# Performance work log

Hardware: AMD Instinct MI355X
Metric: run time of the kernel (lower is better)

Reference implementation:

```python
import jax, jax.numpy as jnp
import numpy as np


def _spectral_norm(W, u):
    # W: [out, in] (1x1 conv weight flattened), u: [out]
    # one power-iteration step (torch does this under no_grad), then
    # sigma = u' @ W @ v with gradient flowing through W only.
    v = W.T @ u
    v = v / jnp.linalg.norm(v)
    u2 = W @ v
    u2 = u2 / jnp.linalg.norm(u2)
    v = jax.lax.stop_gradient(v)
    u2 = jax.lax.stop_gradient(u2)
    sigma = u2 @ (W @ v)
    return W / sigma


def setup_inputs() -> dict:
    key = jax.random.key(0)
    ks = jax.random.split(key, 8)
    B, C, H, W = 32, 512, 32, 32
    Cq = C // 8  # 64
    x = jax.random.normal(ks[0], (B, C, H, W), dtype=jnp.float32)
    s = 1.0 / np.sqrt(C)
    return {
        "x": x,
        "Wq": jax.random.normal(ks[1], (Cq, C), dtype=jnp.float32) * s,
        "bq": jnp.zeros((Cq,), dtype=jnp.float32),
        "uq": jax.random.normal(ks[2], (Cq,), dtype=jnp.float32),
        "Wk": jax.random.normal(ks[3], (Cq, C), dtype=jnp.float32) * s,
        "bk": jnp.zeros((Cq,), dtype=jnp.float32),
        "uk": jax.random.normal(ks[4], (Cq,), dtype=jnp.float32),
        "Wv": jax.random.normal(ks[5], (C, C), dtype=jnp.float32) * s,
        "bv": jnp.zeros((C,), dtype=jnp.float32),
        "uv": jax.random.normal(ks[6], (C,), dtype=jnp.float32),
        "gamma": jnp.float32(0.5),
    }


def reference(x, Wq, bq, uq, Wk, bk, uk, Wv, bv, uv, gamma):
    B, C, H, W = x.shape
    N = H * W
    f = x.reshape(B, C, N)                                   # [B,C,N]
    # 1x1 conv == channel matmul with spectral-normalized weights
    q = jnp.einsum('oc,bcn->bno', _spectral_norm(Wq, uq), f) + bq          # [B,N,Cq]
    k = jnp.einsum('oc,bcn->bon', _spectral_norm(Wk, uk), f) + bk[:, None]  # [B,Cq,N]
    v = jnp.einsum('oc,bcn->bon', _spectral_norm(Wv, uv), f) + bv[:, None]  # [B,C,N]
    qk = jnp.einsum('bno,bom->bnm', q, k)                    # [B,N,N], no 1/sqrt(d)
    attn = jax.nn.softmax(qk, axis=1)                        # softmax over QUERY axis (dim 1)
    o = jnp.einsum('bcn,bnm->bcm', v, attn).reshape(B, C, H, W)
    return gamma * o + x
```

## Files before the change

### kernel.cpp

```cpp
#include <hip/hip_runtime.h>
#include <hip/hip_bf16.h>

typedef __hip_bfloat16 bf16;
typedef __bf16 bf16x8 __attribute__((ext_vector_type(8)));
typedef float  f32x4  __attribute__((ext_vector_type(4)));
typedef unsigned short u16x8 __attribute__((ext_vector_type(8)));

#define C_IN  512
#define N_SP  1024
#define BATCH 32

__device__ __forceinline__ float ldmix(const void* p, size_t i, int f32) {
    return f32 ? ((const float*)p)[i] : __bfloat162float(((const bf16*)p)[i]);
}
__device__ __forceinline__ void stmix(void* p, size_t i, float v, int f32) {
    if (f32) ((float*)p)[i] = v;
    else     ((bf16*)p)[i] = __float2bfloat16(v);
}
__device__ __forceinline__ unsigned short bfbits(float f) {
    bf16 t = __float2bfloat16(f);
    return *reinterpret_cast<unsigned short*>(&t);
}
__device__ __forceinline__ float bf2f(unsigned short h) {
    union { unsigned u; float f; } c; c.u = ((unsigned)h) << 16; return c.f;
}
__device__ __forceinline__ void ldvec8(const void* W, size_t base, int f32, float v[8]) {
    if (f32) {
        const float4* p = reinterpret_cast<const float4*>((const float*)W + base);
        float4 a = p[0], b = p[1];
        v[0] = a.x; v[1] = a.y; v[2] = a.z; v[3] = a.w;
        v[4] = b.x; v[5] = b.y; v[6] = b.z; v[7] = b.w;
    } else {
        u16x8 h = *reinterpret_cast<const u16x8*>((const bf16*)W + base);
#pragma unroll
        for (int j = 0; j < 8; ++j) v[j] = bf2f(h[j]);
    }
}

__global__ void k_detect(const unsigned short* __restrict__ xh, int* __restrict__ flag)
{
    __shared__ int red[256];
    int tid = threadIdx.x;
    unsigned short h = xh[2 * tid];
    int e = (h >> 7) & 0xFF;
    red[tid] = (e == 0 || (e >= 96 && e <= 159)) ? 1 : 0;
    __syncthreads();
    for (int s = 128; s > 0; s >>= 1) { if (tid < s) red[tid] += red[tid + s]; __syncthreads(); }
    if (tid == 0) *flag = (red[0] < 192) ? 1 : 0;
}

__global__ __launch_bounds__(256) void k_sn1(
    const void* __restrict__ Wq, const void* __restrict__ uq,
    const void* __restrict__ Wk, const void* __restrict__ uk,
    const void* __restrict__ Wv, const void* __restrict__ uv,
    const int* __restrict__ flag, float* __restrict__ tpart)
{
    __shared__ float sh_u[64];
    __shared__ float sh_acc[4][512];
    int f32 = *flag;
    int bx = blockIdx.x;
    const void *W, *u; int oc, slot;
    if (bx == 0)      { W = Wq; u = uq; oc = 0;      slot = 0; }
    else if (bx == 1) { W = Wk; u = uk; oc = 0;      slot = 1; }
    else              { W = Wv; u = uv; oc = bx - 2; slot = bx; }
    int tid = threadIdx.x, wave = tid >> 6, lane = tid & 63;
    if (tid < 64) sh_u[tid] = ldmix(u, oc * 64 + tid, f32);
    __syncthreads();

    float acc[8];
#pragma unroll
    for (int j = 0; j < 8; ++j) acc[j] = 0.f;
    int obase = oc * 64 + wave * 16;
#pragma unroll 4
    for (int i = 0; i < 16; ++i) {
        int o = obase + i;
        float w8[8]; ldvec8(W, (size_t)o * C_IN + lane * 8, f32, w8);
        float uo = sh_u[o - oc * 64];
#pragma unroll
        for (int j = 0; j < 8; ++j) acc[j] += w8[j] * uo;
    }
#pragma unroll
    for (int j = 0; j < 8; ++j) sh_acc[wave][lane * 8 + j] = acc[j];
    __syncthreads();
    for (int c = tid; c < 512; c += 256)
        tpart[(size_t)slot * 512 + c] =
            sh_acc[0][c] + sh_acc[1][c] + sh_acc[2][c] + sh_acc[3][c];
}

__global__ __launch_bounds__(512) void k_sn2(
    const void* __restrict__ Wq, const void* __restrict__ Wk,
    const void* __restrict__ Wv, const int* __restrict__ flag,
    const float* __restrict__ tpart, float* __restrict__ sig)
{
    __shared__ float sh_t[512];
    __shared__ float red[512];
    int f32 = *flag;
    int m = blockIdx.x;
    const void* W; int out, slot0, nch;
    if (m == 0)      { W = Wq; out = 64;  slot0 = 0; nch = 1; }
    else if (m == 1) { W = Wk; out = 64;  slot0 = 1; nch = 1; }
    else             { W = Wv; out = 512; slot0 = 2; nch = 8; }
    int tid = threadIdx.x, wave = tid >> 6, lane = tid & 63;

    float t = 0.f;
    for (int c2 = 0; c2 < nch; ++c2) t += tpart[(size_t)(slot0 + c2) * 512 + tid];
    sh_t[tid] = t;
    red[tid] = t * t;
    __syncthreads();
    for (int s = 256; s > 0; s >>= 1) { if (tid < s) red[tid] += red[tid + s]; __syncthreads(); }
    float t2 = red[0];
    __syncthreads();

    float tl[8];
#pragma unroll
    for (int j = 0; j < 8; ++j) tl[j] = sh_t[lane * 8 + j];

    float s2 = 0.f;
#pragma unroll 2
    for (int o = wave; o < out; o += 8) {
        float w8[8]; ldvec8(W, (size_t)o * C_IN + lane * 8, f32, w8);
        float d = 0.f;
#pragma unroll
        for (int j = 0; j < 8; ++j) d += w8[j] * tl[j];
#pragma unroll
        for (int off = 32; off > 0; off >>= 1) d += __shfl_xor(d, off);
        if (lane == 0) s2 += d * d;
    }
    __syncthreads();
    red[tid] = (lane == 0) ? s2 : 0.f;
    __syncthreads();
    for (int s = 256; s > 0; s >>= 1) { if (tid < s) red[tid] += red[tid + s]; __syncthreads(); }
    if (tid == 0) sig[m] = sqrtf(t2 / red[0]);
}

__global__ __launch_bounds__(256) void k_wscale(
    const void* __restrict__ Wq, const void* __restrict__ bq,
    const void* __restrict__ Wk, const void* __restrict__ bk,
    const void* __restrict__ Wv, const void* __restrict__ bv,
    const float* __restrict__ sig, const int* __restrict__ flag,
    bf16* __restrict__ Wb, bf16* __restrict__ Wlo, float* __restrict__ biasf)
{
    int f32 = *flag;
    int r = blockIdx.x;
    const void *W, *b; int row; float s;
    if (r < 64)       { W = Wq; b = bq; row = r;       s = sig[0]; }
    else if (r < 128) { W = Wk; b = bk; row = r - 64;  s = sig[1]; }
    else              { W = Wv; b = bv; row = r - 128; s = sig[2]; }
    for (int c = threadIdx.x; c < C_IN; c += 256) {
        float w = ldmix(W, (size_t)row * C_IN + c, f32) * s;
        bf16 hi = __float2bfloat16(w);
        Wb[(size_t)r * C_IN + c] = hi;
        if (r < 128)
            Wlo[(size_t)r * C_IN + c] = __float2bfloat16(w - __bfloat162float(hi));
    }
    if (threadIdx.x == 0) biasf[r] = ldmix(b, row, f32);
}

__global__ __launch_bounds__(256) void k_xt(
    const void* __restrict__ x, const int* __restrict__ flag,
    char* __restrict__ SX, int batch0)
{
    __shared__ float tile[64][65];
    int f32 = *flag;
    int z = blockIdx.z;
    int n0 = blockIdx.x * 64, c0 = blockIdx.y * 64;
    size_t xoff = (size_t)(batch0 + z) * C_IN * N_SP;
    bf16* xTh = (bf16*)(SX + (size_t)z * 4194304);
    bf16* xTl = xTh + 524288;
    int tid = threadIdx.x;
#pragma unroll
    for (int i = 0; i < 4; ++i) {
        int idx = tid + i * 256;
        int c = idx >> 4, nq = idx & 15;
#pragma unroll
        for (int t = 0; t < 4; ++t)
            tile[c][nq * 4 + t] = ldmix(x, xoff + (size_t)(c0 + c) * N_SP + n0 + nq * 4 + t, f32);
    }
    __syncthreads();
#pragma unroll
    for (int i = 0; i < 16; ++i) {
        int idx = tid + i * 256;
        int n = idx >> 6, c = idx & 63;
        float v = tile[c][n];
        bf16 hi = __float2bfloat16(v);
        xTh[(size_t)(n0 + n) * C_IN + c0 + c] = hi;
        xTl[(size_t)(n0 + n) * C_IN + c0 + c] = __float2bfloat16(v - __bfloat162float(hi));
    }
}

__global__ __launch_bounds__(256) void k_qkv_v(
    const bf16* __restrict__ Wb, const float* __restrict__ biasf,
    const char* __restrict__ SX, bf16* __restrict__ YV)
{
    __shared__ __bf16 Als[128][40];
    __shared__ __bf16 Bls[128][40];
    int z = blockIdx.z;
    int n0 = blockIdx.x * 128;
    int r0 = 128 + blockIdx.y * 128;
    const bf16* xTh = (const bf16*)(SX + (size_t)z * 4194304);
    bf16* Yv = YV + (size_t)z * 524288;
    int tid = threadIdx.x, wave = tid >> 6, lane = tid & 63, quad = lane >> 4, l16 = lane & 15;
    int wc = (wave >> 1) * 64, wm = (wave & 1) * 64;

    f32x4 acc[4][4];
#pragma unroll
    for (int i = 0; i < 4; ++i)
#pragma unroll
        for (int j = 0; j < 4; ++j) acc[i][j] = (f32x4){0.f, 0.f, 0.f, 0.f};

    for (int k0 = 0; k0 < C_IN; k0 += 32) {
#pragma unroll
        for (int s = 0; s < 2; ++s) {
            int idx = tid + s * 256; int row = idx >> 2, ch = idx & 3;
            *reinterpret_cast<uint4*>(&Als[row][ch * 8]) =
                *reinterpret_cast<const uint4*>(&Wb[(size_t)(r0 + row) * C_IN + k0 + ch * 8]);
            *reinterpret_cast<uint4*>(&Bls[row][ch * 8]) =
                *reinterpret_cast<const uint4*>(&xTh[(size_t)(n0 + row) * C_IN + k0 + ch * 8]);
        }
        __syncthreads();
        bf16x8 a[4], b[4];
#pragma unroll
        for (int i = 0; i < 4; ++i)
            a[i] = *reinterpret_cast<const bf16x8*>(&Als[wc + i * 16 + l16][quad * 8]);
#pragma unroll
        for (int j = 0; j < 4; ++j)
            b[j] = *reinterpret_cast<const bf16x8*>(&Bls[wm + j * 16 + l16][quad * 8]);
#pragma unroll
        for (int i = 0; i < 4; ++i)
#pragma unroll
            for (int j = 0; j < 4; ++j)
                acc[i][j] = __builtin_amdgcn_mfma_f32_16x16x32_bf16(a[i], b[j], acc[i][j], 0, 0, 0);
        __syncthreads();
    }
#pragma unroll
    for (int i = 0; i < 4; ++i)
#pragma unroll
        for (int j = 0; j < 4; ++j)
#pragma unroll
            for (int r = 0; r < 4; ++r) {
                int c = r0 + wc + i * 16 + quad * 4 + r;
                int n = n0 + wm + j * 16 + l16;
                Yv[(size_t)(c - 128) * N_SP + n] = __float2bfloat16(acc[i][j][r] + biasf[c]);
            }
}

__global__ __launch_bounds__(256) void k_qkv_qk(
    const bf16* __restrict__ Wb, const bf16* __restrict__ Wlo,
    const float* __restrict__ biasf, const char* __restrict__ SX,
    bf16* __restrict__ QT, bf16* __restrict__ KT)
{
    __shared__ __bf16 Ah[64][40], Al[64][40], Bh[64][40], Bl[64][40];
    int z = blockIdx.z;
    int n0 = blockIdx.x * 64;
    int m0 = blockIdx.y * 64;
    const bf16* xTh = (const bf16*)(SX + (size_t)z * 4194304);
    const bf16* xTl = xTh + 524288;
    bf16* qt = QT + (size_t)z * 65536;
    bf16* kt = KT + (size_t)z * 65536;
    int tid = threadIdx.x, wave = tid >> 6, lane = tid & 63, quad = lane >> 4, l16 = lane & 15;
    int wmh = (wave >> 1) * 32, wnh = (wave & 1) * 32;

    f32x4 acc[2][2];
#pragma unroll
    for (int i = 0; i < 2; ++i)
#pragma unroll
        for (int j = 0; j < 2; ++j) acc[i][j] = (f32x4){0.f, 0.f, 0.f, 0.f};

    for (int k0 = 0; k0 < C_IN; k0 += 32) {
        int row = tid >> 2, ch = tid & 3;
        *reinterpret_cast<uint4*>(&Ah[row][ch * 8]) =
            *reinterpret_cast<const uint4*>(&Wb[(size_t)(m0 + row) * C_IN + k0 + ch * 8]);
        *reinterpret_cast<uint4*>(&Al[row][ch * 8]) =
            *reinterpret_cast<const uint4*>(&Wlo[(size_t)(m0 + row) * C_IN + k0 + ch * 8]);
        *reinterpret_cast<uint4*>(&Bh[row][ch * 8]) =
            *reinterpret_cast<const uint4*>(&xTh[(size_t)(n0 + row) * C_IN + k0 + ch * 8]);
        *reinterpret_cast<uint4*>(&Bl[row][ch * 8]) =
            *reinterpret_cast<const uint4*>(&xTl[(size_t)(n0 + row) * C_IN + k0 + ch * 8]);
        __syncthreads();
        bf16x8 ah[2], al[2], bh[2], bl[2];
#pragma unroll
        for (int i = 0; i < 2; ++i) {
            ah[i] = *reinterpret_cast<const bf16x8*>(&Ah[wmh + i * 16 + l16][quad * 8]);
            al[i] = *reinterpret_cast<const bf16x8*>(&Al[wmh + i * 16 + l16][quad * 8]);
        }
#pragma unroll
        for (int j = 0; j < 2; ++j) {
            bh[j] = *reinterpret_cast<const bf16x8*>(&Bh[wnh + j * 16 + l16][quad * 8]);
            bl[j] = *reinterpret_cast<const bf16x8*>(&Bl[wnh + j * 16 + l16][quad * 8]);
        }
#pragma unroll
        for (int i = 0; i < 2; ++i)
#pragma unroll
            for (int j = 0; j < 2; ++j) {
                acc[i][j] = __builtin_amdgcn_mfma_f32_16x16x32_bf16(ah[i], bh[j], acc[i][j], 0, 0, 0);
                acc[i][j] = __builtin_amdgcn_mfma_f32_16x16x32_bf16(ah[i], bl[j], acc[i][j], 0, 0, 0);
                acc[i][j] = __builtin_amdgcn_mfma_f32_16x16x32_bf16(al[i], bh[j], acc[i][j], 0, 0, 0);
            }
        __syncthreads();
    }
#pragma unroll
    for (int i = 0; i < 2; ++i)
#pragma unroll
        for (int j = 0; j < 2; ++j) {
            int cbase = m0 + wmh + i * 16 + quad * 4;
            int n = n0 + wnh + j * 16 + l16;
            ushort4 st;
            st.x = bfbits(acc[i][j][0] + biasf[cbase + 0]);
            st.y = bfbits(acc[i][j][1] + biasf[cbase + 1]);
            st.z = bfbits(acc[i][j][2] + biasf[cbase + 2]);
            st.w = bfbits(acc[i][j][3] + biasf[cbase + 3]);
            bf16* dst = (m0 == 0) ? &qt[(size_t)n * 64 + cbase]
                                  : &kt[(size_t)n * 64 + (cbase - 64)];
            *reinterpret_cast<ushort4*>(dst) = st;
        }
}

__global__ __launch_bounds__(256) void k_qk(
    const bf16* __restrict__ QT, const bf16* __restrict__ KT,
    char* __restrict__ SX)
{
    __shared__ __bf16 Als[128][40];
    __shared__ __bf16 Bls[128][40];
    int z = blockIdx.z, m0 = blockIdx.y * 128, n0 = blockIdx.x * 128;
    const bf16* qt = QT + (size_t)z * 65536;
    const bf16* kt = KT + (size_t)z * 65536;
    float* Sf = (float*)(SX + (size_t)z * 4194304);
    int tid = threadIdx.x, wave = tid >> 6, lane = tid & 63, quad = lane >> 4, l16 = lane & 15;
    int wc = (wave >> 1) * 64, wm = (wave & 1) * 64;

    f32x4 acc[4][4];
#pragma unroll
    for (int i = 0; i < 4; ++i)
#pragma unroll
        for (int j = 0; j < 4; ++j) acc[i][j] = (f32x4){0.f, 0.f, 0.f, 0.f};

#pragma unroll
    for (int k0 = 0; k0 < 64; k0 += 32) {
#pragma unroll
        for (int s = 0; s < 2; ++s) {
            int idx = tid + s * 256; int row = idx >> 2, ch = idx & 3;
            *reinterpret_cast<uint4*>(&Als[row][ch * 8]) =
                *reinterpret_cast<const uint4*>(&kt[(size_t)(m0 + row) * 64 + k0 + ch * 8]);
            *reinterpret_cast<uint4*>(&Bls[row][ch * 8]) =
                *reinterpret_cast<const uint4*>(&qt[(size_t)(n0 + row) * 64 + k0 + ch * 8]);
        }
        __syncthreads();
        bf16x8 a[4], b[4];
#pragma unroll
        for (int i = 0; i < 4; ++i)
            a[i] = *reinterpret_cast<const bf16x8*>(&Als[wc + i * 16 + l16][quad * 8]);
#pragma unroll
        for (int j = 0; j < 4; ++j)
            b[j] = *reinterpret_cast<const bf16x8*>(&Bls[wm + j * 16 + l16][quad * 8]);
#pragma unroll
        for (int i = 0; i < 4; ++i)
#pragma unroll
            for (int j = 0; j < 4; ++j)
                acc[i][j] = __builtin_amdgcn_mfma_f32_16x16x32_bf16(a[i], b[j], acc[i][j], 0, 0, 0);
        __syncthreads();
    }
#pragma unroll
    for (int i = 0; i < 4; ++i)
#pragma unroll
        for (int j = 0; j < 4; ++j)
#pragma unroll
            for (int r = 0; r < 4; ++r) {
                int m = m0 + wc + i * 16 + quad * 4 + r;
                int n = n0 + wm + j * 16 + l16;
                Sf[(size_t)m * N_SP + n] = acc[i][j][r];
            }
}

__global__ __launch_bounds__(256) void k_softmax(char* __restrict__ SX)
{
    __shared__ float red[256];
    int z = blockIdx.x >> 10, m = blockIdx.x & 1023;
    float* p = (float*)(SX + (size_t)z * 4194304) + (size_t)m * N_SP;
    bf16* pb = (bf16*)p;
    int tid = threadIdx.x;
    float v0 = p[tid], v1 = p[tid + 256], v2 = p[tid + 512], v3 = p[tid + 768];
    red[tid] = fmaxf(fmaxf(v0, v1), fmaxf(v2, v3));
    __syncthreads();
    for (int s = 128; s > 0; s >>= 1) { if (tid < s) red[tid] = fmaxf(red[tid], red[tid + s]); __syncthreads(); }
    float mx = red[0];
    __syncthreads();
    float d0 = fmaxf(fminf(v0 - mx, 0.f), -80.f);
    float d1 = fmaxf(fminf(v1 - mx, 0.f), -80.f);
    float d2 = fmaxf(fminf(v2 - mx, 0.f), -80.f);
    float d3 = fmaxf(fminf(v3 - mx, 0.f), -80.f);
    float e0 = __expf(d0), e1 = __expf(d1), e2 = __expf(d2), e3 = __expf(d3);
    red[tid] = e0 + e1 + e2 + e3;
    __syncthreads();
    for (int s = 128; s > 0; s >>= 1) { if (tid < s) red[tid] += red[tid + s]; __syncthreads(); }
    float inv = 1.f / red[0];
    pb[tid]       = __float2bfloat16(e0 * inv);
    pb[tid + 256] = __float2bfloat16(e1 * inv);
    pb[tid + 512] = __float2bfloat16(e2 * inv);
    pb[tid + 768] = __float2bfloat16(e3 * inv);
}

__global__ __launch_bounds__(256) void k_out(
    const bf16* __restrict__ YV, const char* __restrict__ SX,
    const void* __restrict__ x, const void* __restrict__ gamma,
    const int* __restrict__ flag, void* __restrict__ out, int batch0)
{
    __shared__ __bf16 Als[128][40];
    __shared__ __bf16 Bls[128][40];
    int f32 = *flag;
    int z = blockIdx.z, c0 = blockIdx.y * 128, m0 = blockIdx.x * 128;
    const bf16* Yv = YV + (size_t)z * 524288;
    const bf16* Pb = (const bf16*)(SX + (size_t)z * 4194304);
    int tid = threadIdx.x, wave = tid >> 6, lane = tid & 63, quad = lane >> 4, l16 = lane & 15;
    int wc = (wave >> 1) * 64, wm = (wave & 1) * 64;

    f32x4 acc[4][4];
#pragma unroll
    for (int i = 0; i < 4; ++i)
#pragma unroll
        for (int j = 0; j < 4; ++j) acc[i][j] = (f32x4){0.f, 0.f, 0.f, 0.f};

    for (int k0 = 0; k0 < N_SP; k0 += 32) {
#pragma unroll
        for (int s = 0; s < 2; ++s) {
            int idx = tid + s * 256; int row = idx >> 2, ch = idx & 3;
            *reinterpret_cast<uint4*>(&Als[row][ch * 8]) =
                *reinterpret_cast<const uint4*>(&Yv[(size_t)(c0 + row) * N_SP + k0 + ch * 8]);
            *reinterpret_cast<uint4*>(&Bls[row][ch * 8]) =
                *reinterpret_cast<const uint4*>(&Pb[(size_t)(m0 + row) * 2048 + k0 + ch * 8]);
        }
        __syncthreads();
        bf16x8 a[4], b[4];
#pragma unroll
        for (int i = 0; i < 4; ++i)
            a[i] = *reinterpret_cast<const bf16x8*>(&Als[wc + i * 16 + l16][quad * 8]);
#pragma unroll
        for (int j = 0; j < 4; ++j)
            b[j] = *reinterpret_cast<const bf16x8*>(&Bls[wm + j * 16 + l16][quad * 8]);
#pragma unroll
        for (int i = 0; i < 4; ++i)
#pragma unroll
            for (int j = 0; j < 4; ++j)
                acc[i][j] = __builtin_amdgcn_mfma_f32_16x16x32_bf16(a[i], b[j], acc[i][j], 0, 0, 0);
        __syncthreads();
    }

    float g = ldmix(gamma, 0, f32);
    const size_t base = (size_t)(batch0 + z) * C_IN * N_SP;
#pragma unroll
    for (int i = 0; i < 4; ++i)
#pragma unroll
        for (int j = 0; j < 4; ++j)
#pragma unroll
            for (int r = 0; r < 4; ++r) {
                int c = c0 + wc + i * 16 + quad * 4 + r;
                int m = m0 + wm + j * 16 + l16;
                size_t o = base + (size_t)c * N_SP + m;
                float v = fmaf(g, acc[i][j][r], ldmix(x, o, f32));
                if (!(v == v)) v = 5555.0f + 1000.0f * f32;
                stmix(out, o, v, f32);
            }
}

__global__ void k_wsfail(float* __restrict__ out, int n)
{
    int i = blockIdx.x * 256 + threadIdx.x;
    if (i < n) out[i] = 7777.0f;
}

extern "C" void kernel_launch(void* const* d_in, const int* in_sizes, int n_in,
                              void* d_out, int out_size, void* d_ws, size_t ws_size,
                              hipStream_t stream)
{
    const void* x  = d_in[0];
    const void* Wq = d_in[1];
    const void* bq = d_in[2];
    const void* Wk = d_in[4];
    const void* bk = d_in[5];
    const void* Wv = d_in[7];
    const void* bv = d_in[8];
    const void* uq = d_in[3];
    const void* uk = d_in[6];
    const void* uv = d_in[9];
    const void* gm = d_in[10];

    const size_t HDR = 790528;
    const size_t per = 4194304 + 131072 + 131072 + 1048576;
    int GB = 0;
    for (int g = 32; g >= 1; g >>= 1)
        if (HDR + (size_t)g * per <= ws_size) { GB = g; break; }
    if (GB == 0) {
        k_wsfail<<<(out_size + 255) / 256, 256, 0, stream>>>((float*)d_out, out_size);
        return;
    }
    char* ws = (char*)d_ws;
    int*   flag  = (int*)ws;
    float* sig   = (float*)(ws + 16);
    float* biasf = (float*)(ws + 256);
    bf16*  Wb    = (bf16*)(ws + 4096);
    bf16*  Wlo   = (bf16*)(ws + 659456);
    char*  SX    = ws + HDR;
    bf16*  QT    = (bf16*)(SX + (size_t)GB * 4194304);
    bf16*  KT    = QT + (size_t)GB * 65536;
    bf16*  YV    = KT + (size_t)GB * 65536;
    float* tpart = (float*)SX;

    k_detect<<<1, 256, 0, stream>>>((const unsigned short*)x, flag);
    k_sn1<<<10, 256, 0, stream>>>(Wq, uq, Wk, uk, Wv, uv, flag, tpart);
    k_sn2<<<3, 512, 0, stream>>>(Wq, Wk, Wv, flag, tpart, sig);
    k_wscale<<<640, 256, 0, stream>>>(Wq, bq, Wk, bk, Wv, bv, sig, flag, Wb, Wlo, biasf);
    for (int b0 = 0; b0 < BATCH; b0 += GB) {
        k_xt     <<<dim3(16, 8, GB), 256, 0, stream>>>(x, flag, SX, b0);
        k_qkv_v  <<<dim3(8, 4, GB), 256, 0, stream>>>(Wb, biasf, SX, YV);
        k_qkv_qk <<<dim3(16, 2, GB), 256, 0, stream>>>(Wb, Wlo, biasf, SX, QT, KT);
        k_qk     <<<dim3(8, 8, GB), 256, 0, stream>>>(QT, KT, SX);
        k_softmax<<<GB * 1024, 256, 0, stream>>>(SX);
        k_out    <<<dim3(8, 4, GB), 256, 0, stream>>>(YV, SX, x, gm, flag, d_out, b0);
    }
}
```

Measured before the change: 434.9 us.

## Double-buffer LDS tiles with register prefetch and remap blocks across XCDs

Converts the three MFMA GEMM kernels (v projection, q/k projection, output) to double-buffered shared-memory tiles. The next k-slice is prefetched into registers while the current one is consumed, so only one barrier per iteration is needed instead of two. It also flattens the grid to 1D and decodes block ids so that consecutive blocks with the same tile index land on different XCDs while a batch's tiles stay grouped, aiming for better L2 reuse. The cost is doubled LDS per block, which may lower occupancy, plus higher register pressure from the prefetch registers.

```diff
diff --git a/kernel.cpp b/kernel.cpp
--- a/kernel.cpp
+++ b/kernel.cpp
@@ -34,6 +34,24 @@
         u16x8 h = *reinterpret_cast<const u16x8*>((const bf16*)W + base);
 #pragma unroll
         for (int j = 0; j < 8; ++j) v[j] = bf2f(h[j]);
+    }
+}
+
+__device__ __forceinline__ void lds_barrier() {
+    asm volatile("s_waitcnt lgkmcnt(0)" ::: "memory");
+    __builtin_amdgcn_sched_barrier(0);
+    __builtin_amdgcn_s_barrier();
+    __builtin_amdgcn_sched_barrier(0);
+}
+
+__device__ __forceinline__ void tile_decode(int bid, int nblk, int& z, int& mc) {
+    int GBk = nblk >> 5;
+    if ((GBk & 7) == 0) {
+        z  = (bid & 7) + 8 * ((bid >> 3) >> 5);
+        mc = (bid >> 3) & 31;
+    } else {
+        z  = bid >> 5;
+        mc = bid & 31;
     }
 }
 
@@ -192,15 +210,16 @@
     const bf16* __restrict__ Wb, const float* __restrict__ biasf,
     const char* __restrict__ SX, bf16* __restrict__ YV)
 {
-    __shared__ __bf16 Als[128][40];
-    __shared__ __bf16 Bls[128][40];
-    int z = blockIdx.z;
-    int n0 = blockIdx.x * 128;
-    int r0 = 128 + blockIdx.y * 128;
+    __shared__ __bf16 Als[2][128][40];
+    __shared__ __bf16 Bls[2][128][40];
+    int z, mc; tile_decode(blockIdx.x, gridDim.x, z, mc);
+    int n0 = (mc >> 2) * 128;
+    int r0 = 128 + (mc & 3) * 128;
     const bf16* xTh = (const bf16*)(SX + (size_t)z * 4194304);
     bf16* Yv = YV + (size_t)z * 524288;
     int tid = threadIdx.x, wave = tid >> 6, lane = tid & 63, quad = lane >> 4, l16 = lane & 15;
     int wc = (wave >> 1) * 64, wm = (wave & 1) * 64;
+    int row0 = tid >> 2, row1 = row0 + 64, ch = tid & 3;
 
     f32x4 acc[4][4];
 #pragma unroll
@@ -208,30 +227,36 @@
 #pragma unroll
         for (int j = 0; j < 4; ++j) acc[i][j] = (f32x4){0.f, 0.f, 0.f, 0.f};
 
-    for (int k0 = 0; k0 < C_IN; k0 += 32) {
-#pragma unroll
-        for (int s = 0; s < 2; ++s) {
-            int idx = tid + s * 256; int row = idx >> 2, ch = idx & 3;
-            *reinterpret_cast<uint4*>(&Als[row][ch * 8]) =
-                *reinterpret_cast<const uint4*>(&Wb[(size_t)(r0 + row) * C_IN + k0 + ch * 8]);
-            *reinterpret_cast<uint4*>(&Bls[row][ch * 8]) =
-                *reinterpret_cast<const uint4*>(&xTh[(size_t)(n0 + row) * C_IN + k0 + ch * 8]);
-        }
-        __syncthreads();
+    uint4 ra0, ra1, rb0, rb1;
+#define LDV(t_) { int k0 = (t_) * 32; \
+    ra0 = *reinterpret_cast<const uint4*>(&Wb[(size_t)(r0 + row0) * C_IN + k0 + ch * 8]); \
+    ra1 = *reinterpret_cast<const uint4*>(&Wb[(size_t)(r0 + row1) * C_IN + k0 + ch * 8]); \
+    rb0 = *reinterpret_cast<const uint4*>(&xTh[(size_t)(n0 + row0) * C_IN + k0 + ch * 8]); \
+    rb1 = *reinterpret_cast<const uint4*>(&xTh[(size_t)(n0 + row1) * C_IN + k0 + ch * 8]); }
+    LDV(0);
+#pragma unroll 2
+    for (int t = 0; t < 16; ++t) {
+        int cur = t & 1;
+        *reinterpret_cast<uint4*>(&Als[cur][row0][ch * 8]) = ra0;
+        *reinterpret_cast<uint4*>(&Als[cur][row1][ch * 8]) = ra1;
+        *reinterpret_cast<uint4*>(&Bls[cur][row0][ch * 8]) = rb0;
+        *reinterpret_cast<uint4*>(&Bls[cur][row1][ch * 8]) = rb1;
+        if (t + 1 < 16) LDV(t + 1);
+        lds_barrier();
         bf16x8 a[4], b[4];
 #pragma unroll
         for (int i = 0; i < 4; ++i)
-            a[i] = *reinterpret_cast<const bf16x8*>(&Als[wc + i * 16 + l16][quad * 8]);
+            a[i] = *reinterpret_cast<const bf16x8*>(&Als[cur][wc + i * 16 + l16][quad * 8]);
 #pragma unroll
         for (int j = 0; j < 4; ++j)
-            b[j] = *reinterpret_cast<const bf16x8*>(&Bls[wm + j * 16 + l16][quad * 8]);
+            b[j] = *reinterpret_cast<const bf16x8*>(&Bls[cur][wm + j * 16 + l16][quad * 8]);
 #pragma unroll
         for (int i = 0; i < 4; ++i)
 #pragma unroll
             for (int j = 0; j < 4; ++j)
                 acc[i][j] = __builtin_amdgcn_mfma_f32_16x16x32_bf16(a[i], b[j], acc[i][j], 0, 0, 0);
-        __syncthreads();
-    }
+    }
+#undef LDV
 #pragma unroll
     for (int i = 0; i < 4; ++i)
 #pragma unroll
@@ -249,16 +274,17 @@
     const float* __restrict__ biasf, const char* __restrict__ SX,
     bf16* __restrict__ QT, bf16* __restrict__ KT)
 {
-    __shared__ __bf16 Ah[64][40], Al[64][40], Bh[64][40], Bl[64][40];
-    int z = blockIdx.z;
-    int n0 = blockIdx.x * 64;
-    int m0 = blockIdx.y * 64;
+    __shared__ __bf16 Ah[2][64][40], Al[2][64][40], Bh[2][64][40], Bl[2][64][40];
+    int z, mc; tile_decode(blockIdx.x, gridDim.x, z, mc);
+    int n0 = (mc >> 1) * 64;
+    int m0 = (mc & 1) * 64;
     const bf16* xTh = (const bf16*)(SX + (size_t)z * 4194304);
     const bf16* xTl = xTh + 524288;
     bf16* qt = QT + (size_t)z * 65536;
     bf16* kt = KT + (size_t)z * 65536;
     int tid = threadIdx.x, wave = tid >> 6, lane = tid & 63, quad = lane >> 4, l16 = lane & 15;
     int wmh = (wave >> 1) * 32, wnh = (wave & 1) * 32;
+    int row = tid >> 2, ch = tid & 3;
 
     f32x4 acc[2][2];
 #pragma unroll
@@ -266,38 +292,43 @@
 #pragma unroll
         for (int j = 0; j < 2; ++j) acc[i][j] = (f32x4){0.f, 0.f, 0.f, 0.f};
 
-    for (int k0 = 0; k0 < C_IN; k0 += 32) {
-        int row = tid >> 2, ch = tid & 3;
-        *reinterpret_cast<uint4*>(&Ah[row][ch * 8]) =
-            *reinterpret_cast<const uint4*>(&Wb[(size_t)(m0 + row) * C_IN + k0 + ch * 8]);
-        *reinterpret_cast<uint4*>(&Al[row][ch * 8]) =
-            *reinterpret_cast<const uint4*>(&Wlo[(size_t)(m0 + row) * C_IN + k0 + ch * 8]);
-        *reinterpret_cast<uint4*>(&Bh[row][ch * 8]) =
-            *reinterpret_cast<const uint4*>(&xTh[(size_t)(n0 + row) * C_IN + k0 + ch * 8]);
-        *reinterpret_cast<uint4*>(&Bl[row][ch * 8]) =
-            *reinterpret_cast<const uint4*>(&xTl[(size_t)(n0 + row) * C_IN + k0 + ch * 8]);
-        __syncthreads();
-        bf16x8 ah[2], al[2], bh[2], bl[2];
+    uint4 rah, ral, rbh, rbl;
+#define LDQK(t_) { int k0 = (t_) * 32; \
+    rah = *reinterpret_cast<const uint4*>(&Wb [(size_t)(m0 + row) * C_IN + k0 + ch * 8]); \
+    ral = *reinterpret_cast<const uint4*>(&Wlo[(size_t)(m0 + row) * C_IN + k0 + ch * 8]); \
+    rbh = *reinterpret_cast<const uint4*>(&xTh[(size_t)(n0 + row) * C_IN + k0 + ch * 8]); \
+    rbl = *reinterpret_cast<const uint4*>(&xTl[(size_t)(n0 + row) * C_IN + k0 + ch * 8]); }
+    LDQK(0);
+#pragma unroll 2
+    for (int t = 0; t < 16; ++t) {
+        int cur = t & 1;
+        *reinterpret_cast<uint4*>(&Ah[cur][row][ch * 8]) = rah;
+        *reinterpret_cast<uint4*>(&Al[cur][row][ch * 8]) = ral;
+        *reinterpret_cast<uint4*>(&Bh[cur][row][ch * 8]) = rbh;
+        *reinterpret_cast<uint4*>(&Bl[cur][row][ch * 8]) = rbl;
+        if (t + 1 < 16) LDQK(t + 1);
+        lds_barrier();
+        bf16x8 ah[2], al2[2], bh[2], bl[2];
 #pragma unroll
         for (int i = 0; i < 2; ++i) {
-            ah[i] = *reinterpret_cast<const bf16x8*>(&Ah[wmh + i * 16 + l16][quad * 8]);
-            al[i] = *reinterpret_cast<const bf16x8*>(&Al[wmh + i * 16 + l16][quad * 8]);
+            ah[i]  = *reinterpret_cast<const bf16x8*>(&Ah[cur][wmh + i * 16 + l16][quad * 8]);
+            al2[i] = *reinterpret_cast<const bf16x8*>(&Al[cur][wmh + i * 16 + l16][quad * 8]);
         }
 #pragma unroll
         for (int j = 0; j < 2; ++j) {
-            bh[j] = *reinterpret_cast<const bf16x8*>(&Bh[wnh + j * 16 + l16][quad * 8]);
-            bl[j] = *reinterpret_cast<const bf16x8*>(&Bl[wnh + j * 16 + l16][quad * 8]);
+            bh[j] = *reinterpret_cast<const bf16x8*>(&Bh[cur][wnh + j * 16 + l16][quad * 8]);
+            bl[j] = *reinterpret_cast<const bf16x8*>(&Bl[cur][wnh + j * 16 + l16][quad * 8]);
         }
 #pragma unroll
         for (int i = 0; i < 2; ++i)
 #pragma unroll
             for (int j = 0; j < 2; ++j) {
-                acc[i][j] = __builtin_amdgcn_mfma_f32_16x16x32_bf16(ah[i], bh[j], acc[i][j], 0, 0, 0);
-                acc[i][j] = __builtin_amdgcn_mfma_f32_16x16x32_bf16(ah[i], bl[j], acc[i][j], 0, 0, 0);
-                acc[i][j] = __builtin_amdgcn_mfma_f32_16x16x32_bf16(al[i], bh[j], acc[i][j], 0, 0, 0);
+                acc[i][j] = __builtin_amdgcn_mfma_f32_16x16x32_bf16(ah[i],  bh[j], acc[i][j], 0, 0, 0);
+                acc[i][j] = __builtin_amdgcn_mfma_f32_16x16x32_bf16(ah[i],  bl[j], acc[i][j], 0, 0, 0);
+                acc[i][j] = __builtin_amdgcn_mfma_f32_16x16x32_bf16(al2[i], bh[j], acc[i][j], 0, 0, 0);
             }
-        __syncthreads();
-    }
+    }
+#undef LDQK
 #pragma unroll
     for (int i = 0; i < 2; ++i)
 #pragma unroll
@@ -404,14 +435,16 @@
     const void* __restrict__ x, const void* __restrict__ gamma,
     const int* __restrict__ flag, void* __restrict__ out, int batch0)
 {
-    __shared__ __bf16 Als[128][40];
-    __shared__ __bf16 Bls[128][40];
+    __shared__ __bf16 Als[2][128][40];
+    __shared__ __bf16 Bls[2][128][40];
     int f32 = *flag;
-    int z = blockIdx.z, c0 = blockIdx.y * 128, m0 = blockIdx.x * 128;
+    int z, mc; tile_decode(blockIdx.x, gridDim.x, z, mc);
+    int m0 = (mc >> 2) * 128, c0 = (mc & 3) * 128;
     const bf16* Yv = YV + (size_t)z * 524288;
     const bf16* Pb = (const bf16*)(SX + (size_t)z * 4194304);
     int tid = threadIdx.x, wave = tid >> 6, lane = tid & 63, quad = lane >> 4, l16 = lane & 15;
     int wc = (wave >> 1) * 64, wm = (wave & 1) * 64;
+    int row0 = tid >> 2, row1 = row0 + 64, ch = tid & 3;
 
     f32x4 acc[4][4];
 #pragma unroll
@@ -419,30 +452,36 @@
 #pragma unroll
         for (int j = 0; j < 4; ++j) acc[i][j] = (f32x4){0.f, 0.f, 0.f, 0.f};
 
-    for (int k0 = 0; k0 < N_SP; k0 += 32) {
-#pragma unroll
-        for (int s = 0; s < 2; ++s) {
-            int idx = tid + s * 256; int row = idx >> 2, ch = idx & 3;
-            *reinterpret_cast<uint4*>(&Als[row][ch * 8]) =
-                *reinterpret_cast<const uint4*>(&Yv[(size_t)(c0 + row) * N_SP + k0 + ch * 8]);
-            *reinterpret_cast<uint4*>(&Bls[row][ch * 8]) =
-                *reinterpret_cast<const uint4*>(&Pb[(size_t)(m0 + row) * 2048 + k0 + ch * 8]);
-        }
-        __syncthreads();
+    uint4 ra0, ra1, rb0, rb1;
+#define LDO(t_) { int k0 = (t_) * 32; \
+    ra0 = *reinterpret_cast<const uint4*>(&Yv[(size_t)(c0 + row0) * N_SP + k0 + ch * 8]); \
+    ra1 = *reinterpret_cast<const uint4*>(&Yv[(size_t)(c0 + row1) * N_SP + k0 + ch * 8]); \
+    rb0 = *reinterpret_cast<const uint4*>(&Pb[(size_t)(m0 + row0) * 2048 + k0 + ch * 8]); \
+    rb1 = *reinterpret_cast<const uint4*>(&Pb[(size_t)(m0 + row1) * 2048 + k0 + ch * 8]); }
+    LDO(0);
+#pragma unroll 2
+    for (int t = 0; t < 32; ++t) {
+        int cur = t & 1;
+        *reinterpret_cast<uint4*>(&Als[cur][row0][ch * 8]) = ra0;
+        *reinterpret_cast<uint4*>(&Als[cur][row1][ch * 8]) = ra1;
+        *reinterpret_cast<uint4*>(&Bls[cur][row0][ch * 8]) = rb0;
+        *reinterpret_cast<uint4*>(&Bls[cur][row1][ch * 8]) = rb1;
+        if (t + 1 < 32) LDO(t + 1);
+        lds_barrier();
         bf16x8 a[4], b[4];
 #pragma unroll
         for (int i = 0; i < 4; ++i)
-            a[i] = *reinterpret_cast<const bf16x8*>(&Als[wc + i * 16 + l16][quad * 8]);
+            a[i] = *reinterpret_cast<const bf16x8*>(&Als[cur][wc + i * 16 + l16][quad * 8]);
 #pragma unroll
         for (int j = 0; j < 4; ++j)
-            b[j] = *reinterpret_cast<const bf16x8*>(&Bls[wm + j * 16 + l16][quad * 8]);
+            b[j] = *reinterpret_cast<const bf16x8*>(&Bls[cur][wm + j * 16 + l16][quad * 8]);
 #pragma unroll
         for (int i = 0; i < 4; ++i)
 #pragma unroll
             for (int j = 0; j < 4; ++j)
                 acc[i][j] = __builtin_amdgcn_mfma_f32_16x16x32_bf16(a[i], b[j], acc[i][j], 0, 0, 0);
-        __syncthreads();
-    }
+    }
+#undef LDO
 
     float g = ldmix(gamma, 0, f32);
     const size_t base = (size_t)(batch0 + z) * C_IN * N_SP;
@@ -510,10 +549,10 @@
     k_wscale<<<640, 256, 0, stream>>>(Wq, bq, Wk, bk, Wv, bv, sig, flag, Wb, Wlo, biasf);
     for (int b0 = 0; b0 < BATCH; b0 += GB) {
         k_xt     <<<dim3(16, 8, GB), 256, 0, stream>>>(x, flag, SX, b0);
-        k_qkv_v  <<<dim3(8, 4, GB), 256, 0, stream>>>(Wb, biasf, SX, YV);
-        k_qkv_qk <<<dim3(16, 2, GB), 256, 0, stream>>>(Wb, Wlo, biasf, SX, QT, KT);
+        k_qkv_v  <<<GB * 32, 256, 0, stream>>>(Wb, biasf, SX, YV);
+        k_qkv_qk <<<GB * 32, 256, 0, stream>>>(Wb, Wlo, biasf, SX, QT, KT);
         k_qk     <<<dim3(8, 8, GB), 256, 0, stream>>>(QT, KT, SX);
         k_softmax<<<GB * 1024, 256, 0, stream>>>(SX);
-        k_out    <<<dim3(8, 4, GB), 256, 0, stream>>>(YV, SX, x, gm, flag, d_out, b0);
-    }
-}
+        k_out    <<<GB * 32, 256, 0, stream>>>(YV, SX, x, gm, flag, d_out, b0);
+    }
+}
```

Measured after the change: 409.0 us. 1.06x faster.
